# Performance work log

Hardware: AMD Instinct MI355X
Metric: run time of the kernel (lower is better)

## Reference

```python
import jax, jax.numpy as jnp
import numpy as np


def setup_inputs() -> dict:
    key = jax.random.key(0)
    k1, k2, k3 = jax.random.split(key, 3)
    B, S, D_in, D_out, R = 4, 4096, 4096, 4096, 16
    x = jax.random.normal(k1, (B, S, D_in), dtype=jnp.float32)
    lora_A = jax.random.normal(k2, (R, D_in), dtype=jnp.float32)
    lora_B = jax.random.normal(k3, (D_out, R), dtype=jnp.float32)
    return {"x": x, "lora_A": lora_A, "lora_B": lora_B}


def reference(x, lora_A, lora_B):
    # Faithful to original: materialize W = lora_B @ lora_A (out, in),
    # then F.linear(x, W) == x @ W.T
    W = lora_B @ lora_A  # [out, in]
    return jnp.einsum("bsi,oi->bso", x, W)
```

## Files before the change

kernel.cpp:

```cpp
#include <hip/hip_runtime.h>


typedef float f4 __attribute__((ext_vector_type(4)));

#define M_TOTAL 16384
#define K_DIM 4096
#define N_DIM 4096
#define R_DIM 16

__device__ float t_buf[M_TOTAL * R_DIM];


#define KC 256
#define NCHUNK (K_DIM / KC)

#define LDS_BARRIER() asm volatile("s_waitcnt lgkmcnt(0)\n\ts_barrier" ::: "memory")

__global__ __launch_bounds__(256, 2)
void lora_phase1(const float* __restrict__ x, const float* __restrict__ A)
{
    __shared__ float A_lds[2][R_DIM][KC];

    const int tid  = threadIdx.x;
    const int wave = tid >> 6;
    const int lane = tid & 63;
    const int wave_row0 = blockIdx.x * 16 + wave * 4;

    float acc[4][R_DIM];
    #pragma unroll
    for (int w = 0; w < 4; ++w)
        #pragma unroll
        for (int r = 0; r < R_DIM; ++r) acc[w][r] = 0.0f;

    const f4* xr0 = reinterpret_cast<const f4*>(x + (size_t)(wave_row0 + 0) * K_DIM);
    const f4* xr1 = reinterpret_cast<const f4*>(x + (size_t)(wave_row0 + 1) * K_DIM);
    const f4* xr2 = reinterpret_cast<const f4*>(x + (size_t)(wave_row0 + 2) * K_DIM);
    const f4* xr3 = reinterpret_cast<const f4*>(x + (size_t)(wave_row0 + 3) * K_DIM);

    f4 sreg[4];
    #pragma unroll
    for (int p = 0; p < 4; ++p)
        sreg[p] = *reinterpret_cast<const f4*>(A + (size_t)(p * 4 + wave) * K_DIM + lane * 4);

    f4 xv0 = __builtin_nontemporal_load(&xr0[lane]);
    f4 xv1 = __builtin_nontemporal_load(&xr1[lane]);
    f4 xv2 = __builtin_nontemporal_load(&xr2[lane]);
    f4 xv3 = __builtin_nontemporal_load(&xr3[lane]);

    #pragma unroll
    for (int p = 0; p < 4; ++p)
        *reinterpret_cast<f4*>(&A_lds[0][p * 4 + wave][lane * 4]) = sreg[p];
    LDS_BARRIER();

    #pragma unroll 1
    for (int c = 0; c < NCHUNK; ++c) {
        const int cur = c & 1;
        const bool more = (c + 1 < NCHUNK);
        f4 xn0, xn1, xn2, xn3;
        if (more) {
            #pragma unroll
            for (int p = 0; p < 4; ++p)
                sreg[p] = *reinterpret_cast<const f4*>(
                    A + (size_t)(p * 4 + wave) * K_DIM + (c + 1) * KC + lane * 4);
            const int nidx = (c + 1) * 64 + lane;
            xn0 = __builtin_nontemporal_load(&xr0[nidx]);
            xn1 = __builtin_nontemporal_load(&xr1[nidx]);
            xn2 = __builtin_nontemporal_load(&xr2[nidx]);
            xn3 = __builtin_nontemporal_load(&xr3[nidx]);
        }

        #pragma unroll
        for (int r = 0; r < R_DIM; ++r) {
            f4 av = *reinterpret_cast<const f4*>(&A_lds[cur][r][lane * 4]);
            acc[0][r] += xv0[0] * av[0] + xv0[1] * av[1] + xv0[2] * av[2] + xv0[3] * av[3];
            acc[1][r] += xv1[0] * av[0] + xv1[1] * av[1] + xv1[2] * av[2] + xv1[3] * av[3];
            acc[2][r] += xv2[0] * av[0] + xv2[1] * av[1] + xv2[2] * av[2] + xv2[3] * av[3];
            acc[3][r] += xv3[0] * av[0] + xv3[1] * av[1] + xv3[2] * av[2] + xv3[3] * av[3];
        }

        if (more) {
            #pragma unroll
            for (int p = 0; p < 4; ++p)
                *reinterpret_cast<f4*>(&A_lds[cur ^ 1][p * 4 + wave][lane * 4]) = sreg[p];
            xv0 = xn0; xv1 = xn1; xv2 = xn2; xv3 = xn3;
        }
        LDS_BARRIER();
    }

    #pragma unroll
    for (int w = 0; w < 4; ++w) {
        #pragma unroll
        for (int r = 0; r < R_DIM; ++r) {
            float v = acc[w][r];
            v += __shfl_xor(v, 32, 64);
            v += __shfl_xor(v, 16, 64);
            v += __shfl_xor(v,  8, 64);
            v += __shfl_xor(v,  4, 64);
            v += __shfl_xor(v,  2, 64);
            v += __shfl_xor(v,  1, 64);
            acc[w][r] = v;
        }
    }
    if (lane == 0) {
        #pragma unroll
        for (int w = 0; w < 4; ++w) {
            float* tp = t_buf + (size_t)(wave_row0 + w) * R_DIM;
            #pragma unroll
            for (int rc = 0; rc < 4; ++rc) {
                f4 v = { acc[w][rc * 4 + 0], acc[w][rc * 4 + 1],
                         acc[w][rc * 4 + 2], acc[w][rc * 4 + 3] };
                *reinterpret_cast<f4*>(tp + rc * 4) = v;
            }
        }
    }
}


#define P2_ROWS 64

__global__ __launch_bounds__(256, 2)
void lora_phase2(const float* __restrict__ Bm, float* __restrict__ out)
{
    __shared__ float t_lds[P2_ROWS][R_DIM];

    const int tid  = threadIdx.x;
    const int row0 = (blockIdx.x >> 2) * P2_ROWS;
    const int o0   = (blockIdx.x & 3) * 1024 + tid * 4;

    reinterpret_cast<f4*>(&t_lds[0][0])[tid] =
        reinterpret_cast<const f4*>(t_buf + (size_t)row0 * R_DIM)[tid];

    float br[4][R_DIM];
    #pragma unroll
    for (int oo = 0; oo < 4; ++oo) {
        const f4* bp = reinterpret_cast<const f4*>(Bm + (size_t)(o0 + oo) * R_DIM);
        #pragma unroll
        for (int rc = 0; rc < 4; ++rc) {
            f4 b4 = bp[rc];
            br[oo][rc * 4 + 0] = b4[0];
            br[oo][rc * 4 + 1] = b4[1];
            br[oo][rc * 4 + 2] = b4[2];
            br[oo][rc * 4 + 3] = b4[3];
        }
    }
    __syncthreads();

    #pragma unroll 4
    for (int m = 0; m < P2_ROWS; ++m) {
        float tv[R_DIM];
        const f4* tp = reinterpret_cast<const f4*>(&t_lds[m][0]);
        #pragma unroll
        for (int rc = 0; rc < 4; ++rc) {
            f4 t4 = tp[rc];
            tv[rc * 4 + 0] = t4[0];
            tv[rc * 4 + 1] = t4[1];
            tv[rc * 4 + 2] = t4[2];
            tv[rc * 4 + 3] = t4[3];
        }
        f4 oa = {0.0f, 0.0f, 0.0f, 0.0f};
        #pragma unroll
        for (int r = 0; r < R_DIM; ++r) {
            oa[0] += tv[r] * br[0][r];
            oa[1] += tv[r] * br[1][r];
            oa[2] += tv[r] * br[2][r];
            oa[3] += tv[r] * br[3][r];
        }
        *reinterpret_cast<f4*>(out + (size_t)(row0 + m) * N_DIM + o0) = oa;
    }
}

extern "C" void kernel_launch(void* const* d_in, const int* in_sizes, int n_in,
                              void* d_out, int out_size, void* d_ws, size_t ws_size,
                              hipStream_t stream) {
    const float* x  = (const float*)d_in[0];
    const float* A  = (const float*)d_in[1];
    const float* Bm = (const float*)d_in[2];
    float* out = (float*)d_out;

    lora_phase1<<<dim3(M_TOTAL / 16), dim3(256), 0, stream>>>(x, A);
    lora_phase2<<<dim3((M_TOTAL / P2_ROWS) * 4), dim3(256), 0, stream>>>(Bm, out);
}
```

Before: 462.5 us.

## Fuse LoRA down and up projections into one kernel via LDS

Merges the two kernels into one. Each block computes its 16 rows of x·Aᵀ, keeps the result in shared memory instead of a global scratch buffer, then loops over all output columns to write x·Aᵀ·Bᵀ directly. This removes one kernel launch, the global round-trip of the intermediate, and lets the output stores of one block overlap the reads of others. In exchange every block now reloads all of B (256 KB, likely L2-resident) and holds extra registers across the second stage, which can lower occupancy.

Measured after the change: 743.4 us. 60.7% more time.

```diff
diff --git a/kernel.cpp b/kernel.cpp
--- a/kernel.cpp
+++ b/kernel.cpp
@@ -8,23 +8,23 @@
 #define N_DIM 4096
 #define R_DIM 16
 
-__device__ float t_buf[M_TOTAL * R_DIM];
-
-
 #define KC 256
 #define NCHUNK (K_DIM / KC)
 
 #define LDS_BARRIER() asm volatile("s_waitcnt lgkmcnt(0)\n\ts_barrier" ::: "memory")
 
 __global__ __launch_bounds__(256, 2)
-void lora_phase1(const float* __restrict__ x, const float* __restrict__ A)
+void lora_fused(const float* __restrict__ x, const float* __restrict__ A,
+                const float* __restrict__ Bm, float* __restrict__ out)
 {
     __shared__ float A_lds[2][R_DIM][KC];
+    __shared__ float t_lds[16][R_DIM];
 
     const int tid  = threadIdx.x;
     const int wave = tid >> 6;
     const int lane = tid & 63;
-    const int wave_row0 = blockIdx.x * 16 + wave * 4;
+    const int block_row0 = blockIdx.x * 16;
+    const int wave_row0  = block_row0 + wave * 4;
 
     float acc[4][R_DIM];
     #pragma unroll
@@ -103,69 +103,53 @@
     }
     if (lane == 0) {
         #pragma unroll
-        for (int w = 0; w < 4; ++w) {
-            float* tp = t_buf + (size_t)(wave_row0 + w) * R_DIM;
+        for (int w = 0; w < 4; ++w)
             #pragma unroll
-            for (int rc = 0; rc < 4; ++rc) {
-                f4 v = { acc[w][rc * 4 + 0], acc[w][rc * 4 + 1],
-                         acc[w][rc * 4 + 2], acc[w][rc * 4 + 3] };
-                *reinterpret_cast<f4*>(tp + rc * 4) = v;
-            }
-        }
-    }
-}
-
-
-#define P2_ROWS 64
-
-__global__ __launch_bounds__(256, 2)
-void lora_phase2(const float* __restrict__ Bm, float* __restrict__ out)
-{
-    __shared__ float t_lds[P2_ROWS][R_DIM];
-
-    const int tid  = threadIdx.x;
-    const int row0 = (blockIdx.x >> 2) * P2_ROWS;
-    const int o0   = (blockIdx.x & 3) * 1024 + tid * 4;
-
-    reinterpret_cast<f4*>(&t_lds[0][0])[tid] =
-        reinterpret_cast<const f4*>(t_buf + (size_t)row0 * R_DIM)[tid];
-
-    float br[4][R_DIM];
-    #pragma unroll
-    for (int oo = 0; oo < 4; ++oo) {
-        const f4* bp = reinterpret_cast<const f4*>(Bm + (size_t)(o0 + oo) * R_DIM);
-        #pragma unroll
-        for (int rc = 0; rc < 4; ++rc) {
-            f4 b4 = bp[rc];
-            br[oo][rc * 4 + 0] = b4[0];
-            br[oo][rc * 4 + 1] = b4[1];
-            br[oo][rc * 4 + 2] = b4[2];
-            br[oo][rc * 4 + 3] = b4[3];
-        }
+            for (int r = 0; r < R_DIM; ++r)
+                t_lds[wave * 4 + w][r] = acc[w][r];
     }
     __syncthreads();
 
-    #pragma unroll 4
-    for (int m = 0; m < P2_ROWS; ++m) {
-        float tv[R_DIM];
-        const f4* tp = reinterpret_cast<const f4*>(&t_lds[m][0]);
+    #pragma unroll 1
+    for (int ot = 0; ot < N_DIM / 1024; ++ot) {
+        const int o0 = ot * 1024 + tid * 4;
+
+        float br[4][R_DIM];
         #pragma unroll
-        for (int rc = 0; rc < 4; ++rc) {
-            f4 t4 = tp[rc];
-            tv[rc * 4 + 0] = t4[0];
-            tv[rc * 4 + 1] = t4[1];
-            tv[rc * 4 + 2] = t4[2];
-            tv[rc * 4 + 3] = t4[3];
+        for (int oo = 0; oo < 4; ++oo) {
+            const f4* bp = reinterpret_cast<const f4*>(Bm + (size_t)(o0 + oo) * R_DIM);
+            #pragma unroll
+            for (int rc = 0; rc < 4; ++rc) {
+                f4 b4 = bp[rc];
+                br[oo][rc * 4 + 0] = b4[0];
+                br[oo][rc * 4 + 1] = b4[1];
+                br[oo][rc * 4 + 2] = b4[2];
+                br[oo][rc * 4 + 3] = b4[3];
+            }
         }
-        f4 oa = {0.0f, 0.0f, 0.0f, 0.0f};
+
         #pragma unroll
-        for (int r = 0; r < R_DIM; ++r) {
-            oa[0] += tv[r] * br[0][r];
-            oa[1] += tv[r] * br[1][r];
-            oa[2] += tv[r] * br[2][r];
-            oa[3] += tv[r] * br[3][r];
+        for (int m = 0; m < 16; ++m) {
+            float tv[R_DIM];
+            const f4* tp = reinterpret_cast<const f4*>(&t_lds[m][0]);
+            #pragma unroll
+            for (int rc = 0; rc < 4; ++rc) {
+                f4 t4 = tp[rc];
+                tv[rc * 4 + 0] = t4[0];
+                tv[rc * 4 + 1] = t4[1];
+                tv[rc * 4 + 2] = t4[2];
+                tv[rc * 4 + 3] = t4[3];
+            }
+            f4 oa = {0.0f, 0.0f, 0.0f, 0.0f};
+            #pragma unroll
+            for (int r = 0; r < R_DIM; ++r) {
+                oa[0] += tv[r] * br[0][r];
+                oa[1] += tv[r] * br[1][r];
+                oa[2] += tv[r] * br[2][r];
+                oa[3] += tv[r] * br[3][r];
+            }
+            *reinterpret_cast<f4*>(out + (size_t)(block_row0 + m) * N_DIM + o0) = oa;
         }
-        *reinterpret_cast<f4*>(out + (size_t)(row0 + m) * N_DIM + o0) = oa;
     }
 }
 
@@ -177,6 +161,5 @@
     const float* Bm = (const float*)d_in[2];
     float* out = (float*)d_out;
 
-    lora_phase1<<<dim3(M_TOTAL / 16), dim3(256), 0, stream>>>(x, A);
-    lora_phase2<<<dim3((M_TOTAL / P2_ROWS) * 4), dim3(256), 0, stream>>>(Bm, out);
+    lora_fused<<<dim3(M_TOTAL / 16), dim3(256), 0, stream>>>(x, A, Bm, out);
 }
```
